# Kernel optimization log

Measured on AMD Instinct MI355X. Metric: run time of the kernel, lower is better.

Reference implementation:

```python
import jax, jax.numpy as jnp
import numpy as np

N_HEADS = 16
D_KV = 64
NUM_BUCKETS = 32
MAX_DISTANCE = 128


def _relative_position_bucket(rel_pos, bidirectional=True, num_buckets=NUM_BUCKETS, max_distance=MAX_DISTANCE):
    # rel_pos: int32 [q, k] = key_pos - query_pos
    if bidirectional:
        num_buckets //= 2
        buckets = (rel_pos > 0).astype(jnp.int32) * num_buckets
        rel = jnp.abs(rel_pos)
    else:
        buckets = jnp.zeros_like(rel_pos)
        rel = -jnp.minimum(rel_pos, 0)
    max_exact = num_buckets // 2
    is_small = rel < max_exact
    # log-spaced buckets for large distances (guard log(0) with max(rel,1))
    rel_f = jnp.maximum(rel, 1).astype(jnp.float32)
    large = max_exact + (
        jnp.log(rel_f / max_exact) / np.log(max_distance / max_exact) * (num_buckets - max_exact)
    ).astype(jnp.int32)
    large = jnp.minimum(large, num_buckets - 1)
    return buckets + jnp.where(is_small, rel, large)


def compute_position_bias(rel_bias, q_len, k_len, bidirectional=True):
    # rel_bias: [num_buckets, n_heads] embedding table
    ctx = jnp.arange(q_len, dtype=jnp.int32)[:, None]
    mem = jnp.arange(k_len, dtype=jnp.int32)[None, :]
    buckets = _relative_position_bucket(mem - ctx, bidirectional=bidirectional)  # [q, k]
    values = rel_bias[buckets]                       # [q, k, h]
    return jnp.transpose(values, (2, 0, 1))[None]    # [1, h, q, k]


def setup_inputs() -> dict:
    key = jax.random.key(0)
    ks = jax.random.split(key, 6)
    B, S, D = 4, 1024, 1024
    scale = 0.02
    return {
        "hidden_states": jax.random.normal(ks[0], (B, S, D), jnp.float32),
        "attention_mask": jnp.zeros((1, 1, S, S), jnp.float32),
        "wq": jax.random.normal(ks[1], (D, D), jnp.float32) * scale,
        "wk": jax.random.normal(ks[2], (D, D), jnp.float32) * scale,
        "wv": jax.random.normal(ks[3], (D, D), jnp.float32) * scale,
        "wo": jax.random.normal(ks[4], (D, D), jnp.float32) * scale,
        "rel_bias": jax.random.normal(ks[5], (NUM_BUCKETS, N_HEADS), jnp.float32) * scale,
    }


def reference(hidden_states, attention_mask, wq, wk, wv, wo, rel_bias):
    B, S, D = hidden_states.shape
    H, dk = N_HEADS, D_KV

    def split_heads(x):  # [B, S, H*dk] -> [B, H, S, dk]
        return x.reshape(B, S, H, dk).transpose(0, 2, 1, 3)

    q = split_heads(hidden_states @ wq)
    k = split_heads(hidden_states @ wk)
    v = split_heads(hidden_states @ wv)

    # T5 attention: NO 1/sqrt(dk) scaling
    scores = jnp.einsum("bhqd,bhkd->bhqk", q, k)
    position_bias = compute_position_bias(rel_bias, S, S, bidirectional=True)
    position_bias = position_bias + attention_mask  # additive mask folded into bias
    scores = scores + position_bias

    attn = jax.nn.softmax(scores.astype(jnp.float32), axis=-1).astype(scores.dtype)
    out = jnp.einsum("bhqk,bhkd->bhqd", attn, v)
    out = out.transpose(0, 2, 1, 3).reshape(B, S, H * dk)
    return out @ wo
```

## Files before the change

kernel.cpp:

```cpp
#include <hip/hip_runtime.h>

typedef __attribute__((ext_vector_type(8))) short short8v;
typedef __attribute__((ext_vector_type(4))) short short4v;
typedef __attribute__((ext_vector_type(4))) float floatx4;
typedef __attribute__((ext_vector_type(16))) float f32x16;
typedef __attribute__((ext_vector_type(4))) unsigned uint4v;
typedef __attribute__((ext_vector_type(2))) unsigned uint2v;

#define S_LEN 1024
#define DMODEL 1024
#define NH 16
#define DK 64
#define NB_TAB 2047

__device__ __forceinline__ short f2bf(float f) {
  unsigned u = __builtin_bit_cast(unsigned, f);
  u += 0x7fffu + ((u >> 16) & 1u);
  return (short)(u >> 16);
}

__device__ __forceinline__ unsigned cvtpk(float lo, float hi) {
  unsigned r;
  asm("v_cvt_pk_bf16_f32 %0, %1, %2" : "=v"(r) : "v"(lo), "v"(hi));
  return r;
}

__device__ __forceinline__ void pswap(unsigned& x, unsigned& y) {
  asm volatile("v_permlane32_swap_b32 %0, %1" : "+v"(x), "+v"(y));
}

__device__ __forceinline__ void load16(const void* g, void* l) {
  __builtin_amdgcn_global_load_lds((const __attribute__((address_space(1))) unsigned*)g,
                                   (__attribute__((address_space(3))) unsigned*)l, 16, 0, 0);
}

__global__ __launch_bounds__(256) void transpose4_k(const float* __restrict__ wq,
                                                    const float* __restrict__ wk,
                                                    const float* __restrict__ wv,
                                                    const float* __restrict__ wo,
                                                    short* __restrict__ wT,
                                                    short* __restrict__ wTo) {
  __shared__ float t[32][33];
  int z = blockIdx.z;
  const float* in = z == 0 ? wq : (z == 1 ? wk : (z == 2 ? wv : wo));
  short* out = z < 3 ? wT + (size_t)z * 1024 * 1024 : wTo;
  int tx = threadIdx.x, ty = threadIdx.y;
  int bx = blockIdx.x * 32, by = blockIdx.y * 32;
#pragma unroll
  for (int i = ty; i < 32; i += 8) t[i][tx] = in[(size_t)(by + i) * DMODEL + bx + tx];
  __syncthreads();
#pragma unroll
  for (int i = ty; i < 32; i += 8) out[(size_t)(bx + i) * DMODEL + by + tx] = f2bf(t[tx][i]);
}

__global__ __launch_bounds__(256) void cvt_k(const float* __restrict__ in,
                                             short* __restrict__ out) {
  size_t i = ((size_t)blockIdx.x * 256 + threadIdx.x) * 8;
  const floatx4* p = (const floatx4*)(in + i);
  floatx4 a = p[0], b = p[1];
  short8v o;
#pragma unroll
  for (int j = 0; j < 4; ++j) {
    o[j] = f2bf(a[j]);
    o[4 + j] = f2bf(b[j]);
  }
  *(short8v*)(out + i) = o;
}

__global__ void bias_k(const float* __restrict__ rel_bias, float* __restrict__ tab) {
  int i = blockIdx.x * 256 + threadIdx.x;
  if (i >= NH * NB_TAB) return;
  int h = i / NB_TAB, j = i % NB_TAB;
  int rel = j - 1023;
  int bucket = (rel > 0) ? 16 : 0;
  int r = rel < 0 ? -rel : rel;
  int b;
  if (r < 8) {
    b = r;
  } else {
    float lf = logf((float)r * 0.125f) * (8.0f / 2.772588722239781f);
    b = 8 + (int)lf;
    if (b > 15) b = 15;
  }
  bucket += b;
  tab[i] = rel_bias[bucket * NH + h];
}

__global__ __launch_bounds__(256) void vtrans_k(const short* __restrict__ V,
                                                short* __restrict__ Vt) {
  __shared__ short t[64 * 256];
  int tid = threadIdx.x;
  int s0 = blockIdx.x * 256;
  int bh = blockIdx.y;
#pragma unroll
  for (int i = 0; i < 8; ++i) {
    int s = i * 32 + (tid >> 3);
    int slot = tid & 7;
    short8v vv = *(const short8v*)&V[(((size_t)bh * S_LEN) + s0 + s) * DK + slot * 8];
#pragma unroll
    for (int j = 0; j < 8; ++j) {
      int d = slot * 8 + j;
      *(short*)((char*)t + d * 512 + ((s * 2) ^ (((d >> 3) & 7) << 4))) = vv[j];
    }
  }
  __syncthreads();
#pragma unroll
  for (int i = 0; i < 8; ++i) {
    int d = i * 8 + (tid >> 5);
    int sl = tid & 31;
    short8v vv = *(const short8v*)((char*)t + d * 512 + ((sl * 16) ^ (((d >> 3) & 7) << 4)));
    *(short8v*)&Vt[(((size_t)bh * DK) + d) * S_LEN + s0 + sl * 8] = vv;
  }
}

template <int EPI>
__global__ __launch_bounds__(256) void gemm2_k(const short* __restrict__ A,
                                               const short* __restrict__ BT,
                                               short* __restrict__ Qo, short* __restrict__ Ko,
                                               short* __restrict__ Vo, float* __restrict__ Fo) {
  constexpr int K = DMODEL;
  __shared__ short lA[128 * 64];
  __shared__ short lB[128 * 64];
  int tid = threadIdx.x;
  int lane = tid & 63, wid = tid >> 6;
  int lane16 = lane & 15, kl = lane >> 4;
  int bm = blockIdx.y * 128, bn = blockIdx.x * 128;
  int wm = (wid & 1) * 64, wn = (wid >> 1) * 64;
  floatx4 acc[4][4] = {};

  const char* gA[4];
  const char* gB[4];
  int slot = lane & 7;
#pragma unroll
  for (int it = 0; it < 4; ++it) {
    int row = it * 32 + wid * 8 + (lane >> 3);
    int sw = (slot * 16) ^ ((row & 7) << 4);
    gA[it] = (const char*)A + ((size_t)(bm + row) * K) * 2 + sw;
    gB[it] = (const char*)BT + ((size_t)(bn + row) * K) * 2 + sw;
  }

  for (int k0 = 0; k0 < K; k0 += 64) {
    __syncthreads();
#pragma unroll
    for (int it = 0; it < 4; ++it) {
      char* la = (char*)lA + (it * 32 + wid * 8) * 128;
      char* lb = (char*)lB + (it * 32 + wid * 8) * 128;
      load16(gA[it] + k0 * 2, la);
      load16(gB[it] + k0 * 2, lb);
    }
    __syncthreads();
#pragma unroll
    for (int kc = 0; kc < 2; ++kc) {
      short8v af[4], bf[4];
#pragma unroll
      for (int mt = 0; mt < 4; ++mt) {
        int row = wm + mt * 16 + lane16;
        af[mt] = *(const short8v*)((char*)lA + row * 128 +
                                   ((kc * 64 + kl * 16) ^ ((row & 7) << 4)));
      }
#pragma unroll
      for (int nt = 0; nt < 4; ++nt) {
        int row = wn + nt * 16 + lane16;
        bf[nt] = *(const short8v*)((char*)lB + row * 128 +
                                   ((kc * 64 + kl * 16) ^ ((row & 7) << 4)));
      }
#pragma unroll
      for (int mt = 0; mt < 4; ++mt)
#pragma unroll
        for (int nt = 0; nt < 4; ++nt)
          acc[mt][nt] =
              __builtin_amdgcn_mfma_f32_16x16x32_bf16(af[mt], bf[nt], acc[mt][nt], 0, 0, 0);
    }
  }
  if constexpr (EPI == 0) {
    int which = bn >> 10;
    int gcb = bn & 1023;
    short* dst = which == 0 ? Qo : (which == 1 ? Ko : Vo);
#pragma unroll
    for (int mt = 0; mt < 4; ++mt)
#pragma unroll
      for (int nt = 0; nt < 4; ++nt)
#pragma unroll
        for (int r = 0; r < 4; ++r) {
          int gr = bm + wm + mt * 16 + kl * 4 + r;
          int gc = gcb + wn + nt * 16 + lane16;
          int hh = gc >> 6, d = gc & 63;
          int bb = gr >> 10, s = gr & 1023;
          dst[(size_t)((bb * 16 + hh) * 1024 + s) * 64 + d] = f2bf(acc[mt][nt][r]);
        }
  } else {
#pragma unroll
    for (int mt = 0; mt < 4; ++mt)
#pragma unroll
      for (int nt = 0; nt < 4; ++nt)
#pragma unroll
        for (int r = 0; r < 4; ++r) {
          int gr = bm + wm + mt * 16 + kl * 4 + r;
          int gc = bn + wn + nt * 16 + lane16;
          Fo[(size_t)gr * DMODEL + gc] = acc[mt][nt][r];
        }
  }
}

__global__ __launch_bounds__(256) void attn32_k(const short* __restrict__ Q,
                                                const short* __restrict__ Kg,
                                                const short* __restrict__ Vt,
                                                const float* __restrict__ mask,
                                                const float* __restrict__ biasTab,
                                                short* __restrict__ O) {
  __shared__ short lK[2][64 * 64];
  __shared__ short lV[2][64 * 64];
  __shared__ float lBias[NB_TAB + 1];
  int tid = threadIdx.x;
  int lane = tid & 63, wid = tid >> 6;
  int l31 = lane & 31, L = lane >> 5;
  int qt = blockIdx.x, bh = blockIdx.y;
  int h = bh & 15, b = bh >> 4;

  int q = qt * 128 + wid * 32 + l31;

  const char* gK[2];
  const char* gV[2];
  int ldst[2];
  {
    int slot = lane & 7;
#pragma unroll
    for (int i = 0; i < 2; ++i) {
      int row = i * 32 + wid * 8 + (lane >> 3);
      int ss = slot ^ ((row ^ (row >> 3)) & 7);
      gK[i] = (const char*)Kg + ((size_t)(bh * S_LEN + row) * DK + ss * 8) * 2;
      gV[i] = (const char*)Vt + ((size_t)(bh * DK + row) * S_LEN + ss * 8) * 2;
      ldst[i] = (i * 32 + wid * 8) * 128;
    }
  }
#pragma unroll
  for (int i = 0; i < 2; ++i) {
    load16(gK[i], (char*)lK[0] + ldst[i]);
    load16(gV[i], (char*)lV[0] + ldst[i]);
  }
  for (int i = tid; i < NB_TAB; i += 256) lBias[i] = biasTab[h * NB_TAB + i];
  const short8v* qp = (const short8v*)(Q + ((size_t)bh * S_LEN + q) * DK);
  short8v qf[4];
#pragma unroll
  for (int ds = 0; ds < 4; ++ds) qf[ds] = qp[ds * 2 + L];

  f32x16 ot[2] = {};
  float m_ = -1e30f, l_ = 0.0f;
  __syncthreads();

  for (int it = 0; it < 16; ++it) {
    int kv0 = it * 64;
    int cur = it & 1;
    floatx4 mv[2][4];
#pragma unroll
    for (int hh = 0; hh < 2; ++hh)
#pragma unroll
      for (int g = 0; g < 4; ++g)
        mv[hh][g] = *(const floatx4*)(mask + (size_t)q * S_LEN + kv0 + hh * 32 + 8 * g + 4 * L);
    if (it < 15) {
#pragma unroll
      for (int i = 0; i < 2; ++i) {
        load16(gK[i] + (size_t)(kv0 + 64) * 128, (char*)lK[cur ^ 1] + ldst[i]);
        load16(gV[i] + (size_t)(kv0 + 64) * 2, (char*)lV[cur ^ 1] + ldst[i]);
      }
    }
    f32x16 sA[2];
#pragma unroll
    for (int hh = 0; hh < 2; ++hh) {
      f32x16 acc = {};
#pragma unroll
      for (int ds = 0; ds < 4; ++ds) {
        int row = hh * 32 + l31;
        int sw = ((row ^ (row >> 3)) & 7) << 4;
        short8v kf =
            *(const short8v*)((const char*)lK[cur] + row * 128 + ((ds * 32 + L * 16) ^ sw));
        acc = __builtin_amdgcn_mfma_f32_32x32x16_bf16(kf, qf[ds], acc, 0, 0, 0);
      }
      sA[hh] = acc;
    }
    float p[2][16];
#pragma unroll
    for (int hh = 0; hh < 2; ++hh)
#pragma unroll
      for (int g = 0; g < 4; ++g) {
        int bi = kv0 + hh * 32 + 8 * g + 4 * L - q + 1023;
        floatx4 mvv = mv[hh][g];
#pragma unroll
        for (int r3 = 0; r3 < 4; ++r3)
          p[hh][4 * g + r3] = sA[hh][4 * g + r3] + lBias[bi + r3] + mvv[r3];
      }
    float pmax = p[0][0];
#pragma unroll
    for (int hh = 0; hh < 2; ++hh)
#pragma unroll
      for (int r = 0; r < 16; ++r) pmax = fmaxf(pmax, p[hh][r]);
    pmax = fmaxf(pmax, __shfl_xor(pmax, 32));
    if (__any(pmax > m_ + 8.0f)) {
      float mn = fmaxf(m_, pmax);
      float al = __expf(m_ - mn);
      m_ = mn;
      l_ *= al;
#pragma unroll
      for (int dt = 0; dt < 2; ++dt) ot[dt] *= al;
    }
    float s = 0.0f;
#pragma unroll
    for (int hh = 0; hh < 2; ++hh)
#pragma unroll
      for (int r = 0; r < 16; ++r) {
        float e = __expf(p[hh][r] - m_);
        p[hh][r] = e;
        s += e;
      }
    s += __shfl_xor(s, 32);
    l_ += s;
#pragma unroll
    for (int ks = 0; ks < 4; ++ks) {
      const int hh = ks >> 1, bq = (ks & 1) * 8;
      unsigned A0 = cvtpk(p[hh][bq + 0], p[hh][bq + 1]);
      unsigned A1 = cvtpk(p[hh][bq + 2], p[hh][bq + 3]);
      unsigned B0 = cvtpk(p[hh][bq + 4], p[hh][bq + 5]);
      unsigned B1 = cvtpk(p[hh][bq + 6], p[hh][bq + 7]);
      pswap(A0, B0);
      pswap(A1, B1);
      uint4v uu = {A0, A1, B0, B1};
      short8v pf = __builtin_bit_cast(short8v, uu);
#pragma unroll
      for (int dt = 0; dt < 2; ++dt) {
        int row = dt * 32 + l31;
        int sw = ((row ^ (row >> 3)) & 7) << 4;
        short8v vf =
            *(const short8v*)((const char*)lV[cur] + row * 128 + ((ks * 32 + L * 16) ^ sw));
        ot[dt] = __builtin_amdgcn_mfma_f32_32x32x16_bf16(vf, pf, ot[dt], 0, 0, 0);
      }
    }
    __syncthreads();
  }
  float inv = 1.0f / l_;
  short* ob = O + ((size_t)(b * S_LEN + q)) * DMODEL + h * 64;
#pragma unroll
  for (int dt = 0; dt < 2; ++dt)
#pragma unroll
    for (int g = 0; g < 4; ++g) {
      int d0 = dt * 32 + 8 * g + 4 * L;
      uint2v w = {cvtpk(ot[dt][4 * g + 0] * inv, ot[dt][4 * g + 1] * inv),
                  cvtpk(ot[dt][4 * g + 2] * inv, ot[dt][4 * g + 3] * inv)};
      *(uint2v*)(ob + d0) = w;
    }
}

extern "C" void kernel_launch(void* const* d_in, const int* in_sizes, int n_in, void* d_out,
                              int out_size, void* d_ws, size_t ws_size, hipStream_t stream) {
  (void)in_sizes;
  (void)n_in;
  (void)out_size;
  (void)ws_size;
  const float* hs = (const float*)d_in[0];
  const float* mask = (const float*)d_in[1];
  const float* wq = (const float*)d_in[2];
  const float* wk = (const float*)d_in[3];
  const float* wv = (const float*)d_in[4];
  const float* wo = (const float*)d_in[5];
  const float* relb = (const float*)d_in[6];
  float* out = (float*)d_out;
  char* ws = (char*)d_ws;
  const size_t MB = 1024 * 1024;
  short* wT = (short*)(ws);
  short* wTo = (short*)(ws + 6 * MB);
  short* Ab = (short*)(ws + 8 * MB);
  short* Qb = (short*)(ws + 16 * MB);
  short* Kb = (short*)(ws + 24 * MB);
  short* Vb = (short*)(ws + 32 * MB);
  short* Vtb = (short*)(ws + 40 * MB);
  float* btab = (float*)(ws + 48 * MB);
  short* Ob = Ab;

  transpose4_k<<<dim3(32, 32, 4), dim3(32, 8), 0, stream>>>(wq, wk, wv, wo, wT, wTo);
  bias_k<<<(NH * NB_TAB + 255) / 256, 256, 0, stream>>>(relb, btab);
  cvt_k<<<4096 * 1024 / 8 / 256, 256, 0, stream>>>(hs, Ab);
  gemm2_k<0><<<dim3(3072 / 128, 4096 / 128), 256, 0, stream>>>(Ab, wT, Qb, Kb, Vb, nullptr);
  vtrans_k<<<dim3(4, 64), 256, 0, stream>>>(Vb, Vtb);
  attn32_k<<<dim3(8, 64), 256, 0, stream>>>(Qb, Kb, Vtb, mask, btab, Ob);
  gemm2_k<1><<<dim3(1024 / 128, 4096 / 128), 256, 0, stream>>>(Ob, wTo, nullptr, nullptr, nullptr,
                                                               out);
}
```

Baseline: 205.6 us.

## Pre-swizzle bf16 mask and packed bias tables, stage via LDS, use exp2

The additive mask is pre-converted to bf16, pre-scaled by log2(e) and stored in an XOR-swizzled layout. The attention kernel then streams it into double-buffered LDS with async global-to-LDS loads instead of per-lane float4 global reads. The relative-position bias table is stored as bf16 groups of four consecutive entries, so each lane gets one vector LDS read instead of scalar loads. Q is pre-scaled by log2(e) so the softmax uses raw v_exp_f32 (exp2), with the rescale threshold widened in base-2 units and split max/sum accumulators. The cost is extra preprocessing kernels, more LDS per block (possibly lower occupancy), and bf16 rounding of the mask and bias values.

```diff
diff --git a/kernel.cpp b/kernel.cpp
--- a/kernel.cpp
+++ b/kernel.cpp
@@ -12,6 +12,7 @@
 #define NH 16
 #define DK 64
 #define NB_TAB 2047
+#define L2E 1.4426950408889634f
 
 __device__ __forceinline__ short f2bf(float f) {
   unsigned u = __builtin_bit_cast(unsigned, f);
@@ -19,6 +20,10 @@
   return (short)(u >> 16);
 }
 
+__device__ __forceinline__ float b2f(short s) {
+  return __builtin_bit_cast(float, ((unsigned)(unsigned short)s) << 16);
+}
+
 __device__ __forceinline__ unsigned cvtpk(float lo, float hi) {
   unsigned r;
   asm("v_cvt_pk_bf16_f32 %0, %1, %2" : "=v"(r) : "v"(lo), "v"(hi));
@@ -27,6 +32,12 @@
 
 __device__ __forceinline__ void pswap(unsigned& x, unsigned& y) {
   asm volatile("v_permlane32_swap_b32 %0, %1" : "+v"(x), "+v"(y));
+}
+
+__device__ __forceinline__ float exp2a(float x) {
+  float r;
+  asm("v_exp_f32 %0, %1" : "=v"(r) : "v"(x));
+  return r;
 }
 
 __device__ __forceinline__ void load16(const void* g, void* l) {
@@ -67,23 +78,49 @@
   *(short8v*)(out + i) = o;
 }
 
-__global__ void bias_k(const float* __restrict__ rel_bias, float* __restrict__ tab) {
-  int i = blockIdx.x * 256 + threadIdx.x;
-  if (i >= NH * NB_TAB) return;
-  int h = i / NB_TAB, j = i % NB_TAB;
-  int rel = j - 1023;
-  int bucket = (rel > 0) ? 16 : 0;
-  int r = rel < 0 ? -rel : rel;
-  int b;
-  if (r < 8) {
-    b = r;
+__global__ __launch_bounds__(256) void bias4_k(const float* __restrict__ rel_bias,
+                                               short* __restrict__ B4) {
+  int gid = blockIdx.x * 256 + threadIdx.x;
+  int h = gid >> 11, idx = gid & 2047;
+  short4v o;
+#pragma unroll
+  for (int j = 0; j < 4; ++j) {
+    int ri = idx + j;
+    if (ri > 2046) ri = 2046;
+    int rel = ri - 1023;
+    int bucket = (rel > 0) ? 16 : 0;
+    int r = rel < 0 ? -rel : rel;
+    int bb;
+    if (r < 8) {
+      bb = r;
+    } else {
+      float lf = logf((float)r * 0.125f) * (8.0f / 2.772588722239781f);
+      bb = 8 + (int)lf;
+      if (bb > 15) bb = 15;
+    }
+    bucket += bb;
+    o[j] = f2bf(rel_bias[bucket * NH + h] * L2E);
+  }
+  *(short4v*)(B4 + (size_t)gid * 4) = o;
+}
+
+__global__ __launch_bounds__(256) void masksw_k(const float* __restrict__ mask,
+                                                short* __restrict__ Msw) {
+  int gid = blockIdx.x * 256 + threadIdx.x;
+  int q = gid >> 7, kvg = gid & 127;
+  int kv = kvg * 8;
+  floatx4 m0 = *(const floatx4*)(mask + (size_t)q * 1024 + kv);
+  floatx4 m1 = *(const floatx4*)(mask + (size_t)q * 1024 + kv + 4);
+  unsigned u0 = cvtpk(m0[0] * L2E, m0[1] * L2E), u1 = cvtpk(m0[2] * L2E, m0[3] * L2E);
+  unsigned u2 = cvtpk(m1[0] * L2E, m1[1] * L2E), u3 = cvtpk(m1[2] * L2E, m1[3] * L2E);
+  uint4v uu;
+  if (q & 8) {
+    uu[0] = u2; uu[1] = u3; uu[2] = u0; uu[3] = u1;
   } else {
-    float lf = logf((float)r * 0.125f) * (8.0f / 2.772588722239781f);
-    b = 8 + (int)lf;
-    if (b > 15) b = 15;
-  }
-  bucket += b;
-  tab[i] = rel_bias[bucket * NH + h];
+    uu[0] = u0; uu[1] = u1; uu[2] = u2; uu[3] = u3;
+  }
+  int seg = kvg >> 3, sslot = (kvg & 7) ^ (q & 7);
+  *(uint4v*)(Msw + (size_t)q * 1024 + seg * 64 + sslot * 8) = uu;
 }
 
 __global__ __launch_bounds__(256) void vtrans_k(const short* __restrict__ V,
@@ -176,6 +213,7 @@
     int which = bn >> 10;
     int gcb = bn & 1023;
     short* dst = which == 0 ? Qo : (which == 1 ? Ko : Vo);
+    float scl = which == 0 ? L2E : 1.0f;
 #pragma unroll
     for (int mt = 0; mt < 4; ++mt)
 #pragma unroll
@@ -186,7 +224,7 @@
           int gc = gcb + wn + nt * 16 + lane16;
           int hh = gc >> 6, d = gc & 63;
           int bb = gr >> 10, s = gr & 1023;
-          dst[(size_t)((bb * 16 + hh) * 1024 + s) * 64 + d] = f2bf(acc[mt][nt][r]);
+          dst[(size_t)((bb * 16 + hh) * 1024 + s) * 64 + d] = f2bf(acc[mt][nt][r] * scl);
         }
   } else {
 #pragma unroll
@@ -205,19 +243,20 @@
 __global__ __launch_bounds__(256) void attn32_k(const short* __restrict__ Q,
                                                 const short* __restrict__ Kg,
                                                 const short* __restrict__ Vt,
-                                                const float* __restrict__ mask,
-                                                const float* __restrict__ biasTab,
+                                                const short* __restrict__ Msw,
+                                                const short* __restrict__ B4g,
                                                 short* __restrict__ O) {
   __shared__ short lK[2][64 * 64];
   __shared__ short lV[2][64 * 64];
-  __shared__ float lBias[NB_TAB + 1];
+  __shared__ short lM[2][128 * 64];
+  __shared__ short lB4[2048 * 4];
   int tid = threadIdx.x;
   int lane = tid & 63, wid = tid >> 6;
   int l31 = lane & 31, L = lane >> 5;
   int qt = blockIdx.x, bh = blockIdx.y;
   int h = bh & 15, b = bh >> 4;
-
   int q = qt * 128 + wid * 32 + l31;
+  int q_r = wid * 32 + l31;
 
   const char* gK[2];
   const char* gV[2];
@@ -233,12 +272,26 @@
       ldst[i] = (i * 32 + wid * 8) * 128;
     }
   }
+  const char* gM[4];
+  int ldstM[4];
+#pragma unroll
+  for (int c = 0; c < 4; ++c) {
+    int row = c * 32 + wid * 8 + (lane >> 3);
+    gM[c] = (const char*)Msw + ((size_t)(qt * 128 + row) * 1024) * 2 + (lane & 7) * 16;
+    ldstM[c] = c * 4096 + wid * 1024;
+  }
 #pragma unroll
   for (int i = 0; i < 2; ++i) {
     load16(gK[i], (char*)lK[0] + ldst[i]);
     load16(gV[i], (char*)lV[0] + ldst[i]);
   }
-  for (int i = tid; i < NB_TAB; i += 256) lBias[i] = biasTab[h * NB_TAB + i];
+#pragma unroll
+  for (int c = 0; c < 4; ++c) load16(gM[c], (char*)lM[0] + ldstM[c]);
+  {
+    const short8v* src = (const short8v*)(B4g + (size_t)h * 8192);
+    short8v* dst = (short8v*)lB4;
+    for (int i = tid; i < 1024; i += 256) dst[i] = src[i];
+  }
   const short8v* qp = (const short8v*)(Q + ((size_t)bh * S_LEN + q) * DK);
   short8v qf[4];
 #pragma unroll
@@ -246,24 +299,32 @@
 
   f32x16 ot[2] = {};
   float m_ = -1e30f, l_ = 0.0f;
+  int swq = ((q_r & 7) << 4) | (q_r & 8);
   __syncthreads();
 
   for (int it = 0; it < 16; ++it) {
     int kv0 = it * 64;
     int cur = it & 1;
-    floatx4 mv[2][4];
-#pragma unroll
-    for (int hh = 0; hh < 2; ++hh)
-#pragma unroll
-      for (int g = 0; g < 4; ++g)
-        mv[hh][g] = *(const floatx4*)(mask + (size_t)q * S_LEN + kv0 + hh * 32 + 8 * g + 4 * L);
     if (it < 15) {
 #pragma unroll
       for (int i = 0; i < 2; ++i) {
         load16(gK[i] + (size_t)(kv0 + 64) * 128, (char*)lK[cur ^ 1] + ldst[i]);
         load16(gV[i] + (size_t)(kv0 + 64) * 2, (char*)lV[cur ^ 1] + ldst[i]);
       }
-    }
+#pragma unroll
+      for (int c = 0; c < 4; ++c)
+        load16(gM[c] + (size_t)(kv0 + 64) * 2, (char*)lM[cur ^ 1] + ldstM[c]);
+    }
+    short4v mb[2][4], bb[2][4];
+#pragma unroll
+    for (int hh = 0; hh < 2; ++hh)
+#pragma unroll
+      for (int g = 0; g < 4; ++g) {
+        mb[hh][g] = *(const short4v*)((const char*)lM[cur] + q_r * 128 +
+                                      ((hh * 64 + 16 * g + 8 * L) ^ swq));
+        bb[hh][g] =
+            *(const short4v*)(lB4 + (size_t)(kv0 + hh * 32 + 8 * g + 4 * L - q + 1023) * 4);
+      }
     f32x16 sA[2];
 #pragma unroll
     for (int hh = 0; hh < 2; ++hh) {
@@ -282,36 +343,49 @@
 #pragma unroll
     for (int hh = 0; hh < 2; ++hh)
 #pragma unroll
-      for (int g = 0; g < 4; ++g) {
-        int bi = kv0 + hh * 32 + 8 * g + 4 * L - q + 1023;
-        floatx4 mvv = mv[hh][g];
+      for (int g = 0; g < 4; ++g)
 #pragma unroll
         for (int r3 = 0; r3 < 4; ++r3)
-          p[hh][4 * g + r3] = sA[hh][4 * g + r3] + lBias[bi + r3] + mvv[r3];
-      }
-    float pmax = p[0][0];
+          p[hh][4 * g + r3] = sA[hh][4 * g + r3] + b2f(mb[hh][g][r3]) + b2f(bb[hh][g][r3]);
+    float mx0 = p[0][0], mx1 = p[0][1], mx2 = p[0][2], mx3 = p[0][3];
 #pragma unroll
     for (int hh = 0; hh < 2; ++hh)
 #pragma unroll
-      for (int r = 0; r < 16; ++r) pmax = fmaxf(pmax, p[hh][r]);
+      for (int r = (hh == 0 ? 4 : 0); r < 16; r += 4) {
+        mx0 = fmaxf(mx0, p[hh][r]);
+        mx1 = fmaxf(mx1, p[hh][r + 1]);
+        mx2 = fmaxf(mx2, p[hh][r + 2]);
+        mx3 = fmaxf(mx3, p[hh][r + 3]);
+      }
+    float pmax = fmaxf(fmaxf(mx0, mx1), fmaxf(mx2, mx3));
     pmax = fmaxf(pmax, __shfl_xor(pmax, 32));
-    if (__any(pmax > m_ + 8.0f)) {
+    if (__any(pmax > m_ + 11.5f)) {
       float mn = fmaxf(m_, pmax);
-      float al = __expf(m_ - mn);
+      float al = exp2a(m_ - mn);
       m_ = mn;
       l_ *= al;
 #pragma unroll
       for (int dt = 0; dt < 2; ++dt) ot[dt] *= al;
     }
-    float s = 0.0f;
+    float s0 = 0.0f, s1 = 0.0f, s2 = 0.0f, s3 = 0.0f;
 #pragma unroll
     for (int hh = 0; hh < 2; ++hh)
 #pragma unroll
-      for (int r = 0; r < 16; ++r) {
-        float e = __expf(p[hh][r] - m_);
-        p[hh][r] = e;
-        s += e;
-      }
+      for (int g = 0; g < 4; ++g) {
+        float e0 = exp2a(p[hh][4 * g + 0] - m_);
+        float e1 = exp2a(p[hh][4 * g + 1] - m_);
+        float e2 = exp2a(p[hh][4 * g + 2] - m_);
+        float e3 = exp2a(p[hh][4 * g + 3] - m_);
+        p[hh][4 * g + 0] = e0;
+        p[hh][4 * g + 1] = e1;
+        p[hh][4 * g + 2] = e2;
+        p[hh][4 * g + 3] = e3;
+        s0 += e0;
+        s1 += e1;
+        s2 += e2;
+        s3 += e3;
+      }
+    float s = (s0 + s1) + (s2 + s3);
     s += __shfl_xor(s, 32);
     l_ += s;
 #pragma unroll
@@ -372,15 +446,17 @@
   short* Kb = (short*)(ws + 24 * MB);
   short* Vb = (short*)(ws + 32 * MB);
   short* Vtb = (short*)(ws + 40 * MB);
-  float* btab = (float*)(ws + 48 * MB);
+  short* B4 = (short*)(ws + 48 * MB);
+  short* Msw = (short*)(ws + 49 * MB);
   short* Ob = Ab;
 
   transpose4_k<<<dim3(32, 32, 4), dim3(32, 8), 0, stream>>>(wq, wk, wv, wo, wT, wTo);
-  bias_k<<<(NH * NB_TAB + 255) / 256, 256, 0, stream>>>(relb, btab);
+  bias4_k<<<16 * 2048 / 256, 256, 0, stream>>>(relb, B4);
+  masksw_k<<<1024 * 128 / 256, 256, 0, stream>>>(mask, Msw);
   cvt_k<<<4096 * 1024 / 8 / 256, 256, 0, stream>>>(hs, Ab);
   gemm2_k<0><<<dim3(3072 / 128, 4096 / 128), 256, 0, stream>>>(Ab, wT, Qb, Kb, Vb, nullptr);
   vtrans_k<<<dim3(4, 64), 256, 0, stream>>>(Vb, Vtb);
-  attn32_k<<<dim3(8, 64), 256, 0, stream>>>(Qb, Kb, Vtb, mask, btab, Ob);
+  attn32_k<<<dim3(8, 64), 256, 0, stream>>>(Qb, Kb, Vtb, Msw, B4, Ob);
   gemm2_k<1><<<dim3(1024 / 128, 4096 / 128), 256, 0, stream>>>(Ob, wTo, nullptr, nullptr, nullptr,
                                                                out);
 }
```

Measured after the change: 207.3 us. About the same (+0.8%).
